# Kernel optimization log

Measured on AMD Instinct MI355X. Metric: run time of the kernel, lower is better.

The kernel has to match this reference:

```python
import jax, jax.numpy as jnp
import numpy as np

C, H, W = 256, 56, 56          # feature map dims
N = 128                        # number of proposals
OUT = 7                        # output_size
SCALE = 0.0625                 # spatial_scale = 1/16
K = W // OUT + 2               # max adaptive-pool bin extent (safe upper bound)
NEG = jnp.float32(-3.4e38)


def setup_inputs() -> dict:
    key = jax.random.key(0)
    k1, k2, k3, k4, k5 = jax.random.split(key, 5)
    feature_map = jax.random.normal(k1, (C, H, W), dtype=jnp.float32)
    img = W / SCALE  # 896 px image
    x1 = jax.random.uniform(k2, (N,), minval=0.0, maxval=0.65 * img)
    y1 = jax.random.uniform(k3, (N,), minval=0.0, maxval=0.65 * img)
    bw = jax.random.uniform(k4, (N,), minval=0.12 * img, maxval=0.33 * img)
    bh = jax.random.uniform(k5, (N,), minval=0.12 * img, maxval=0.33 * img)
    proposals = jnp.stack([x1, y1, x1 + bw, y1 + bh], axis=1).astype(jnp.float32)
    return {"feature_map": feature_map, "proposals": proposals}


def _bins(lo, length, out_size, kmax):
    """Adaptive-pool bin indices. PyTorch adaptive pooling: bin i covers
    [floor(i*L/out), ceil((i+1)*L/out)). Returns idx [N,out,K] and mask [N,out,K]."""
    i = jnp.arange(out_size)
    start = (i[None, :] * length[:, None]) // out_size                 # floor div
    end = -((-(i[None, :] + 1) * length[:, None]) // out_size)         # ceil div
    k = jnp.arange(kmax)
    idx = lo[:, None, None] + start[:, :, None] + k[None, None, :]
    mask = k[None, None, :] < (end - start)[:, :, None]
    return idx, mask


def _roi_pool(feature_map, proposals):
    # int(coord*scale): coords are non-negative so Python int() == floor
    boxes = jnp.floor(proposals * SCALE).astype(jnp.int32)
    x1 = jnp.maximum(boxes[:, 0], 0)
    y1 = jnp.maximum(boxes[:, 1], 0)
    x2 = jnp.minimum(boxes[:, 2], W)
    y2 = jnp.minimum(boxes[:, 3], H)
    rw = x2 - x1  # roi widths  (>=1 by construction)
    rh = y2 - y1  # roi heights (>=1 by construction)

    # --- max over width bins (separable max) ---
    idx_w, m_w = _bins(x1, rw, OUT, K)            # [N,OUT,K]
    idx_w = jnp.clip(idx_w, 0, W - 1)
    g = feature_map[:, :, idx_w]                  # [C,H,N,OUT,K]
    colmax = jnp.where(m_w[None, None], g, NEG).max(axis=-1)  # [C,H,N,OUT]

    # --- max over height bins ---
    idx_h, m_h = _bins(y1, rh, OUT, K)            # [N,OUT,K]
    idx_h = jnp.clip(idx_h, 0, H - 1)
    n_idx = jnp.arange(N)[:, None, None]
    g2 = colmax[:, idx_h, n_idx, :]               # [C,N,OUT,K,OUT]
    pooled = jnp.where(m_h[None, :, :, :, None], g2, NEG).max(axis=3)  # [C,N,OUT,OUT]

    return jnp.transpose(pooled, (1, 0, 2, 3))    # [N,C,OUT,OUT], matches torch.stack


def reference(feature_map, proposals):
    return _roi_pool(feature_map, proposals)
```

## Files before the change

kernel.cpp:

```cpp
#include <hip/hip_runtime.h>
#include <stdint.h>


constexpr int Cc = 256, Hh = 56, Ww = 56, OUTS = 7;
constexpr int CHW = Hh * Ww;
constexpr float SCALEF = 0.0625f;
constexpr float NEGF = -3.4e+38f;
constexpr int RH     = 20;
constexpr int RWQ    = 6;
constexpr int PITCHF = 24;
constexpr int BUFF   = 512;
constexpr int WPB    = 4;
constexpr int CPW    = 8;

__device__ __forceinline__ void gll16(const float* g, float* l) {
    __builtin_amdgcn_global_load_lds(
        (const __attribute__((address_space(1))) uint32_t*)g,
        (__attribute__((address_space(3))) uint32_t*)l, 16, 0, 0);
}

template <int E>
__device__ __forceinline__ float binmax(const float* __restrict__ base,
                                        int eh, int ew)
{
    float m = NEGF;
#pragma unroll
    for (int kr = 0; kr < E; ++kr) {
        const int ro = min(kr, eh) * PITCHF;
#pragma unroll
        for (int kc = 0; kc < E; ++kc)
            m = fmaxf(m, base[ro + min(kc, ew)]);
    }
    return m;
}

__global__ __launch_bounds__(256) void roipool_kernel(
    const float* __restrict__ fm,
    const float* __restrict__ props,
    float* __restrict__ out)
{
    __shared__ float lds[WPB][2][BUFF];

    const int lane = threadIdx.x & 63;
    const int wid  = __builtin_amdgcn_readfirstlane(threadIdx.x >> 6);
    const int n    = blockIdx.x >> 3;
    const int cg   = blockIdx.x & 7;
    const int c0   = cg * (WPB * CPW) + wid * CPW;

    const float4 p = reinterpret_cast<const float4*>(props)[n];
    const int x1 = __builtin_amdgcn_readfirstlane(max((int)floorf(p.x * SCALEF), 0));
    const int y1 = __builtin_amdgcn_readfirstlane(max((int)floorf(p.y * SCALEF), 0));
    const int x2 = __builtin_amdgcn_readfirstlane(min((int)floorf(p.z * SCALEF), Ww));
    const int y2 = __builtin_amdgcn_readfirstlane(min((int)floorf(p.w * SCALEF), Hh));
    const int rw = x2 - x1;
    const int rh = y2 - y1;

    float* dst0 = out + ((size_t)n * Cc + c0) * (OUTS * OUTS);
    const float* base0 = fm + (size_t)c0 * CHW;
    const int x1a = x1 & ~3;

    if (rw > 0 && rh > 0 && rw <= 20 && rh <= RH &&
        (y1 + rh < Hh || x1a + RWQ * 4 <= Ww)) {

        int EW = 1, EH = 1;
#pragma unroll
        for (int i = 0; i < 7; ++i) {
            EW = max(EW, ((i + 1) * rw + 6) / 7 - (i * rw) / 7);
            EH = max(EH, ((i + 1) * rh + 6) / 7 - (i * rh) / 7);
        }
        const int E = max(EW, EH);

        const int r0 = lane / RWQ,        q0 = lane - r0 * RWQ;
        const int r1 = (lane + 64) / RWQ, q1 = (lane + 64) - r1 * RWQ;
        const int go0 = min(r0, rh - 1) * Ww + q0 * 4;
        const int go1 = min(r1, rh - 1) * Ww + q1 * 4;
        const float* src0 = base0 + y1 * Ww + x1a;

        const int ow = lane % OUTS;
        const int oh = lane / OUTS;
        const int ws = (ow * rw) / OUTS;
        const int ew = ((ow + 1) * rw + 6) / OUTS - ws - 1;
        const int hs = (oh * rh) / OUTS;
        const int eh = ((oh + 1) * rh + 6) / OUTS - hs - 1;
        const int bofs = hs * PITCHF + (x1 - x1a) + ws;

        float* const b0 = &lds[wid][0][0];
        float* const b1 = &lds[wid][1][0];

        gll16(src0 + go0, b0);
        gll16(src0 + go1, b0 + 256);

#pragma unroll
        for (int k = 0; k < CPW; ++k) {
            const float* buf = (k & 1) ? b1 : b0;
            if (k + 1 < CPW) {
                const float* sn = src0 + (k + 1) * CHW;
                float* bn = ((k + 1) & 1) ? b1 : b0;
                gll16(sn + go0, bn);
                gll16(sn + go1, bn + 256);
            }
            if (k == 0)             asm volatile("s_waitcnt vmcnt(2)" ::: "memory");
            else if (k + 1 < CPW)   asm volatile("s_waitcnt vmcnt(3)" ::: "memory");
            else                    asm volatile("s_waitcnt vmcnt(1)" ::: "memory");
            __builtin_amdgcn_sched_barrier(0);

            if (lane < OUTS * OUTS) {
                const float* bb = buf + bofs;
                float m;
                if (E <= 2)      m = binmax<2>(bb, eh, ew);
                else if (E == 3) m = binmax<3>(bb, eh, ew);
                else             m = binmax<4>(bb, eh, ew);
                dst0[k * (OUTS * OUTS) + lane] = m;
            }
        }
    } else {
        if (lane < OUTS * OUTS) {
            const int ow = lane % OUTS;
            const int oh = lane / OUTS;
            for (int k = 0; k < CPW; ++k) {
                float m = NEGF;
                if (rw > 0 && rh > 0) {
                    const int ws = x1 + (ow * rw) / OUTS;
                    const int we = min(x1 + ((ow + 1) * rw + 6) / OUTS, Ww);
                    const int hs = y1 + (oh * rh) / OUTS;
                    const int he = min(y1 + ((oh + 1) * rh + 6) / OUTS, Hh);
                    const float* b = base0 + (size_t)k * CHW;
                    for (int h = hs; h < he; ++h)
                        for (int w = ws; w < we; ++w)
                            m = fmaxf(m, b[h * Ww + w]);
                }
                dst0[k * (OUTS * OUTS) + lane] = m;
            }
        }
    }
}

extern "C" void kernel_launch(void* const* d_in, const int* in_sizes, int n_in,
                              void* d_out, int out_size, void* d_ws, size_t ws_size,
                              hipStream_t stream)
{
    const float* fm    = (const float*)d_in[0];
    const float* props = (const float*)d_in[1];
    float* out = (float*)d_out;

    const int N = in_sizes[1] / 4;
    const int blocks = N * (Cc / (WPB * CPW));
    roipool_kernel<<<blocks, 256, 0, stream>>>(fm, props, out);
}
```

Measured before the change: 13.24 us.

## Replace LDS double-buffered staging with direct global gathers per bin

Drops the global_load_lds double-buffered staging of each ROI tile into shared memory, along with its manual vmcnt waits. Each lane now precomputes its E*E clamped global offsets once and gathers straight from global memory for all 8 channels, with every load issued up front so the memory system and caches supply the parallelism. This removes the LDS traffic and the serialising waits. In exchange, the loads are scattered scalar gathers that depend on L2/L1 hits rather than coalesced 16-byte transfers.

```diff
diff --git a/kernel.cpp b/kernel.cpp
--- a/kernel.cpp
+++ b/kernel.cpp
@@ -6,32 +6,39 @@
 constexpr int CHW = Hh * Ww;
 constexpr float SCALEF = 0.0625f;
 constexpr float NEGF = -3.4e+38f;
-constexpr int RH     = 20;
-constexpr int RWQ    = 6;
-constexpr int PITCHF = 24;
-constexpr int BUFF   = 512;
-constexpr int WPB    = 4;
-constexpr int CPW    = 8;
-
-__device__ __forceinline__ void gll16(const float* g, float* l) {
-    __builtin_amdgcn_global_load_lds(
-        (const __attribute__((address_space(1))) uint32_t*)g,
-        (__attribute__((address_space(3))) uint32_t*)l, 16, 0, 0);
-}
+constexpr int WPB = 4;
+constexpr int CPW = 8;
 
 template <int E>
-__device__ __forceinline__ float binmax(const float* __restrict__ base,
-                                        int eh, int ew)
+__device__ __forceinline__ void run_channels(
+    const float* __restrict__ base0,
+    float* __restrict__ dst0,
+    int x1, int y1, int rw, int rh, int lane)
 {
-    float m = NEGF;
+    const int ow = lane % OUTS;
+    const int oh = lane / OUTS;
+    const int ws = (ow * rw) / OUTS;
+    const int ew = ((ow + 1) * rw + 6) / OUTS - ws - 1;
+    const int hs = (oh * rh) / OUTS;
+    const int eh = ((oh + 1) * rh + 6) / OUTS - hs - 1;
+
+    int ofs[E * E];
 #pragma unroll
-    for (int kr = 0; kr < E; ++kr) {
-        const int ro = min(kr, eh) * PITCHF;
+    for (int kr = 0; kr < E; ++kr)
 #pragma unroll
         for (int kc = 0; kc < E; ++kc)
-            m = fmaxf(m, base[ro + min(kc, ew)]);
+            ofs[kr * E + kc] =
+                (y1 + hs + min(kr, eh)) * Ww + (x1 + ws + min(kc, ew));
+
+#pragma unroll
+    for (int k = 0; k < CPW; ++k) {
+        const float* __restrict__ b = base0 + k * CHW;
+        float m = NEGF;
+#pragma unroll
+        for (int i = 0; i < E * E; ++i)
+            m = fmaxf(m, b[ofs[i]]);
+        dst0[k * (OUTS * OUTS) + lane] = m;
     }
-    return m;
 }
 
 __global__ __launch_bounds__(256) void roipool_kernel(
@@ -39,8 +46,6 @@
     const float* __restrict__ props,
     float* __restrict__ out)
 {
-    __shared__ float lds[WPB][2][BUFF];
-
     const int lane = threadIdx.x & 63;
     const int wid  = __builtin_amdgcn_readfirstlane(threadIdx.x >> 6);
     const int n    = blockIdx.x >> 3;
@@ -57,11 +62,8 @@
 
     float* dst0 = out + ((size_t)n * Cc + c0) * (OUTS * OUTS);
     const float* base0 = fm + (size_t)c0 * CHW;
-    const int x1a = x1 & ~3;
 
-    if (rw > 0 && rh > 0 && rw <= 20 && rh <= RH &&
-        (y1 + rh < Hh || x1a + RWQ * 4 <= Ww)) {
-
+    if (rw > 0 && rh > 0 && rw <= 20 && rh <= 20) {
         int EW = 1, EH = 1;
 #pragma unroll
         for (int i = 0; i < 7; ++i) {
@@ -70,48 +72,10 @@
         }
         const int E = max(EW, EH);
 
-        const int r0 = lane / RWQ,        q0 = lane - r0 * RWQ;
-        const int r1 = (lane + 64) / RWQ, q1 = (lane + 64) - r1 * RWQ;
-        const int go0 = min(r0, rh - 1) * Ww + q0 * 4;
-        const int go1 = min(r1, rh - 1) * Ww + q1 * 4;
-        const float* src0 = base0 + y1 * Ww + x1a;
-
-        const int ow = lane % OUTS;
-        const int oh = lane / OUTS;
-        const int ws = (ow * rw) / OUTS;
-        const int ew = ((ow + 1) * rw + 6) / OUTS - ws - 1;
-        const int hs = (oh * rh) / OUTS;
-        const int eh = ((oh + 1) * rh + 6) / OUTS - hs - 1;
-        const int bofs = hs * PITCHF + (x1 - x1a) + ws;
-
-        float* const b0 = &lds[wid][0][0];
-        float* const b1 = &lds[wid][1][0];
-
-        gll16(src0 + go0, b0);
-        gll16(src0 + go1, b0 + 256);
-
-#pragma unroll
-        for (int k = 0; k < CPW; ++k) {
-            const float* buf = (k & 1) ? b1 : b0;
-            if (k + 1 < CPW) {
-                const float* sn = src0 + (k + 1) * CHW;
-                float* bn = ((k + 1) & 1) ? b1 : b0;
-                gll16(sn + go0, bn);
-                gll16(sn + go1, bn + 256);
-            }
-            if (k == 0)             asm volatile("s_waitcnt vmcnt(2)" ::: "memory");
-            else if (k + 1 < CPW)   asm volatile("s_waitcnt vmcnt(3)" ::: "memory");
-            else                    asm volatile("s_waitcnt vmcnt(1)" ::: "memory");
-            __builtin_amdgcn_sched_barrier(0);
-
-            if (lane < OUTS * OUTS) {
-                const float* bb = buf + bofs;
-                float m;
-                if (E <= 2)      m = binmax<2>(bb, eh, ew);
-                else if (E == 3) m = binmax<3>(bb, eh, ew);
-                else             m = binmax<4>(bb, eh, ew);
-                dst0[k * (OUTS * OUTS) + lane] = m;
-            }
+        if (lane < OUTS * OUTS) {
+            if (E <= 2)      run_channels<2>(base0, dst0, x1, y1, rw, rh, lane);
+            else if (E == 3) run_channels<3>(base0, dst0, x1, y1, rw, rh, lane);
+            else             run_channels<4>(base0, dst0, x1, y1, rw, rh, lane);
         }
     } else {
         if (lane < OUTS * OUTS) {
```

After: 27.11 us. +104.7%, slower.
